# Optimization experiments

Hardware: AMD Instinct MI355X
Metric: run time of the kernel (lower is better)

Reference implementation:

```python
import jax, jax.numpy as jnp
import numpy as np

B, N, E, FIN, H, OUT = 256, 256, 4096, 128, 256, 256
RATIO = 0.5
BN_EPS = 1e-5


def gin_conv(x, src, dst, valid, W1, b1, W2, b2):
    # per-graph: x [n, f], src/dst [E] int, valid [E] bool
    n = x.shape[0]
    v = valid.astype(x.dtype)
    msg = x[jnp.where(valid, src, 0)] * v[:, None]            # [E, f]
    agg = jax.ops.segment_sum(msg, jnp.where(valid, dst, n), num_segments=n + 1)[:n]
    h = x + agg                                               # GINConv eps = 0
    return jax.nn.gelu(h @ W1 + b1) @ W2 + b2


def batch_norm(x, gamma, beta):
    # training-mode BN over all nodes of all graphs: x [B, n, H]
    mean = x.mean(axis=(0, 1))
    var = ((x - mean) ** 2).mean(axis=(0, 1))
    return (x - mean) * jax.lax.rsqrt(var + BN_EPS) * gamma + beta


def topk_pool(x, src, dst, valid, w, k):
    # PyG TopKPooling: score = x.w / ||w||, keep top-k, gate with tanh(score)
    score = (x @ w) / jnp.linalg.norm(w)                      # [n]
    vals, perm = jax.lax.top_k(score, k)
    x_new = x[perm] * jnp.tanh(vals)[:, None]                 # [k, H]
    mapping = jnp.full((x.shape[0],), -1, dtype=jnp.int32).at[perm].set(
        jnp.arange(k, dtype=jnp.int32))
    new_src = mapping[src]
    new_dst = mapping[dst]
    valid_new = valid & (new_src >= 0) & (new_dst >= 0)
    return x_new, new_src, new_dst, valid_new


def block(x, src, dst, valid, W1, b1, W2, b2, gamma, beta, pw):
    x = jax.vmap(gin_conv, in_axes=(0, 0, 0, 0, None, None, None, None))(
        x, src, dst, valid, W1, b1, W2, b2)
    x = jax.nn.gelu(batch_norm(x, gamma, beta))
    k = int(np.ceil(RATIO * x.shape[1]))
    pool = lambda xi, si, di, vi: topk_pool(xi, si, di, vi, pw, k)
    x, src, dst, valid = jax.vmap(pool)(x, src, dst, valid)
    readout = jnp.concatenate([x.max(axis=1), x.mean(axis=1)], axis=-1)  # gmp||gap
    return x, src, dst, valid, readout


def setup_inputs() -> dict:
    key = jax.random.key(0)
    ks = jax.random.split(key, 64)
    d = {}
    d['x'] = jax.random.normal(ks[0], (B, N, FIN), jnp.float32)
    d['edge_index'] = jax.random.randint(ks[1], (B, 2, E), 0, N, dtype=jnp.int32)
    ki = 2
    fin = FIN
    for l in (1, 2, 3, 4):
        d[f'W1_{l}'] = jax.random.normal(ks[ki], (fin, H), jnp.float32) / np.sqrt(fin); ki += 1
        d[f'b1_{l}'] = jnp.zeros((H,), jnp.float32)
        d[f'W2_{l}'] = jax.random.normal(ks[ki], (H, H), jnp.float32) / np.sqrt(H); ki += 1
        d[f'b2_{l}'] = jnp.zeros((H,), jnp.float32)
        d[f'gamma_{l}'] = jnp.ones((H,), jnp.float32)
        d[f'beta_{l}'] = jnp.zeros((H,), jnp.float32)
        d[f'pw_{l}'] = jax.random.normal(ks[ki], (H,), jnp.float32); ki += 1
        fin = H
    d['Wlin'] = jax.random.normal(ks[ki], (2 * H, OUT), jnp.float32) / np.sqrt(2 * H); ki += 1
    d['blin'] = jnp.zeros((OUT,), jnp.float32)
    return d


def reference(x, edge_index,
              W1_1, b1_1, W2_1, b2_1, gamma_1, beta_1, pw_1,
              W1_2, b1_2, W2_2, b2_2, gamma_2, beta_2, pw_2,
              W1_3, b1_3, W2_3, b2_3, gamma_3, beta_3, pw_3,
              W1_4, b1_4, W2_4, b2_4, gamma_4, beta_4, pw_4,
              Wlin, blin):
    src = edge_index[:, 0]
    dst = edge_index[:, 1]
    valid = jnp.ones(src.shape, dtype=bool)
    layers = [
        (W1_1, b1_1, W2_1, b2_1, gamma_1, beta_1, pw_1),
        (W1_2, b1_2, W2_2, b2_2, gamma_2, beta_2, pw_2),
        (W1_3, b1_3, W2_3, b2_3, gamma_3, beta_3, pw_3),
        (W1_4, b1_4, W2_4, b2_4, gamma_4, beta_4, pw_4),
    ]
    total = None
    for p in layers:
        x, src, dst, valid, r = block(x, src, dst, valid, *p)
        total = r if total is None else total + r
    return total @ Wlin + blin
```

## Files before the change

### kernel.cpp

```cpp
#include <hip/hip_runtime.h>
#include <hip/hip_bf16.h>
#include <math.h>

#define BATCH 256
#define NEDGE 4096
#define HDIM 256

typedef __attribute__((ext_vector_type(8))) short short8v;
typedef __attribute__((ext_vector_type(4))) float float4v;

__device__ __forceinline__ float gelu_f(float x) {
  float x3 = x * x * x;
  float t = tanhf(0.7978845608028654f * (x + 0.044715f * x3));
  return 0.5f * x * (1.0f + t);
}

__device__ __forceinline__ void split_bf16(float v, __hip_bfloat16& hi, __hip_bfloat16& lo) {
  hi = __float2bfloat16(v);
  lo = __float2bfloat16(v - __bfloat162float(hi));
}

template<int NN>
__global__ __launch_bounds__(256)
void csr_build_kernel(const int* __restrict__ src_base, int src_stride,
                      const int* __restrict__ dst_base, int dst_stride,
                      int* __restrict__ g_rs,
                      int* __restrict__ g_ids) {
  __shared__ int s_cnt[NN];
  __shared__ int s_rs[NN + 1];
  __shared__ int s_csr[NEDGE];
  const int b = blockIdx.x;
  const int tid = threadIdx.x;
  const int* se = src_base + (size_t)b * src_stride;
  const int* de = dst_base + (size_t)b * dst_stride;
  if (tid < NN) s_cnt[tid] = 0;
  __syncthreads();
  for (int e = tid; e < NEDGE; e += 256) {
    int s = se[e];
    if (s >= 0) atomicAdd(&s_cnt[de[e]], 1);
  }
  __syncthreads();
  if (tid < NN) s_rs[tid] = s_cnt[tid];
  __syncthreads();
  for (int off = 1; off < NN; off <<= 1) {
    int add = 0;
    if (tid < NN && tid >= off) add = s_rs[tid - off];
    __syncthreads();
    if (tid < NN) s_rs[tid] += add;
    __syncthreads();
  }
  int incl = (tid < NN) ? s_rs[tid] : 0;
  __syncthreads();
  if (tid < NN) s_rs[tid + 1] = incl;
  if (tid == 0) s_rs[0] = 0;
  if (tid < NN) s_cnt[tid] = 0;
  __syncthreads();
  for (int e = tid; e < NEDGE; e += 256) {
    int s = se[e];
    if (s >= 0) {
      int d = de[e];
      int p = s_rs[d] + atomicAdd(&s_cnt[d], 1);
      s_csr[p] = s;
    }
  }
  __syncthreads();
  const int total = s_rs[NN];
  for (int i = tid; i <= NN; i += 256) g_rs[b * (NN + 1) + i] = s_rs[i];
  for (int i = tid; i < total; i += 256) g_ids[b * NEDGE + i] = s_csr[i];
}

template<int NN, int FF, int ZS>
__global__ __launch_bounds__(256)
void gin_gather_kernel(const float* __restrict__ x,
                       const int* __restrict__ g_rs, const int* __restrict__ g_ids,
                       __hip_bfloat16* __restrict__ Hhi,
                       __hip_bfloat16* __restrict__ Hlo) {
  constexpr int LPE = 8;
  constexpr int GRP = 256 / LPE;
  constexpr int F4 = FF / 4;
  __shared__ int s_rs[NN + 1];
  __shared__ int s_ids[NEDGE];
  const int b = blockIdx.x;
  const int chunk = blockIdx.y;
  const int tid = threadIdx.x;
  for (int i = tid; i <= NN; i += 256) s_rs[i] = g_rs[b * (NN + 1) + i];
  __syncthreads();
  const int total = s_rs[NN];
  for (int i = tid; i < total; i += 256) s_ids[i] = g_ids[b * NEDGE + i];
  __syncthreads();
  const int lane = tid & (LPE - 1);
  const int grp = tid / LPE;
  const int cb = chunk * LPE;
  const int r0 = blockIdx.z * (NN / ZS);
  const int r1 = r0 + NN / ZS;
  const float4* x4 = (const float4*)x + (size_t)b * NN * F4;
  for (int d = r0 + grp; d < r1; d += GRP) {
    int j0 = s_rs[d], j1 = s_rs[d + 1];
    float4 acc = x4[(size_t)d * F4 + cb + lane];
    for (int j = j0; j < j1; ++j) {
      int s = s_ids[j];
      float4 xv = x4[(size_t)s * F4 + cb + lane];
      acc.x += xv.x; acc.y += xv.y; acc.z += xv.z; acc.w += xv.w;
    }
    float av[4] = {acc.x, acc.y, acc.z, acc.w};
    union { __hip_bfloat16 h[4]; uint2 u; } hv, lv;
#pragma unroll
    for (int j = 0; j < 4; ++j) split_bf16(av[j], hv.h[j], lv.h[j]);
    size_t eo = ((size_t)b * NN + d) * FF + (cb + lane) * 4;
    *(uint2*)&Hhi[eo] = hv.u;
    *(uint2*)&Hlo[eo] = lv.u;
  }
}

template<int K>
__global__ __launch_bounds__(256)
void wsplit_kernel(const float* __restrict__ W,
                   __hip_bfloat16* __restrict__ Whi, __hip_bfloat16* __restrict__ Wlo) {
  int idx = blockIdx.x * 256 + threadIdx.x;
  int c = idx / K, k = idx % K;
  float w = W[(size_t)k * 256 + c];
  __hip_bfloat16 hi, lo;
  split_bf16(w, hi, lo);
  Whi[idx] = hi;
  Wlo[idx] = lo;
}

template<int K, int MODE>
__global__ __launch_bounds__(256)
void mfma_gemm_kernel(const __hip_bfloat16* __restrict__ Ahi,
                      const __hip_bfloat16* __restrict__ Alo,
                      const __hip_bfloat16* __restrict__ Bhi,
                      const __hip_bfloat16* __restrict__ Blo,
                      const float* __restrict__ bias,
                      float* __restrict__ Cf,
                      __hip_bfloat16* __restrict__ Chi,
                      __hip_bfloat16* __restrict__ Clo,
                      float* __restrict__ P1,
                      float* __restrict__ P2) {
  const int tid = threadIdx.x;
  const int wid = tid >> 6, lane = tid & 63;
  const int wr = wid >> 1, wc = wid & 1;
  const int lr = lane & 15, lg = lane >> 4;
  const int rowBase = blockIdx.x * 128 + wr * 64;
  const int colBase = blockIdx.y * 128 + wc * 64;
  float4v acc[4][4];
#pragma unroll
  for (int m = 0; m < 4; ++m)
#pragma unroll
    for (int n = 0; n < 4; ++n) acc[m][n] = (float4v){0.f, 0.f, 0.f, 0.f};
#pragma unroll 2
  for (int k0 = 0; k0 < K; k0 += 32) {
    short8v ah[4], al[4], bh[4], bl[4];
#pragma unroll
    for (int m = 0; m < 4; ++m) {
      size_t off = (size_t)(rowBase + m * 16 + lr) * K + k0 + lg * 8;
      ah[m] = *(const short8v*)(Ahi + off);
      al[m] = *(const short8v*)(Alo + off);
    }
#pragma unroll
    for (int n = 0; n < 4; ++n) {
      size_t off = (size_t)(colBase + n * 16 + lr) * K + k0 + lg * 8;
      bh[n] = *(const short8v*)(Bhi + off);
      bl[n] = *(const short8v*)(Blo + off);
    }
#pragma unroll
    for (int m = 0; m < 4; ++m)
#pragma unroll
      for (int n = 0; n < 4; ++n) {
        acc[m][n] = __builtin_amdgcn_mfma_f32_16x16x32_bf16(ah[m], bh[n], acc[m][n], 0, 0, 0);
        acc[m][n] = __builtin_amdgcn_mfma_f32_16x16x32_bf16(al[m], bh[n], acc[m][n], 0, 0, 0);
        acc[m][n] = __builtin_amdgcn_mfma_f32_16x16x32_bf16(ah[m], bl[n], acc[m][n], 0, 0, 0);
      }
  }
  float s1[4] = {0.f, 0.f, 0.f, 0.f};
  float s2[4] = {0.f, 0.f, 0.f, 0.f};
#pragma unroll
  for (int n = 0; n < 4; ++n) {
    const int col = colBase + n * 16 + lr;
    const float bv = bias[col];
#pragma unroll
    for (int m = 0; m < 4; ++m) {
      const int row0 = rowBase + m * 16 + lg * 4;
#pragma unroll
      for (int i = 0; i < 4; ++i) {
        float o = acc[m][n][i] + bv;
        if (MODE == 1) {
          o = gelu_f(o);
          __hip_bfloat16 hi, lo;
          split_bf16(o, hi, lo);
          Chi[(size_t)(row0 + i) * 256 + col] = hi;
          Clo[(size_t)(row0 + i) * 256 + col] = lo;
        } else {
          Cf[(size_t)(row0 + i) * 256 + col] = o;
          s1[n] += o;
          s2[n] += o * o;
        }
      }
    }
  }
  if constexpr (MODE == 0) {
    __shared__ float r1[128][8];
    __shared__ float r2[128][8];
    const int slot = wr * 4 + lg;
#pragma unroll
    for (int n = 0; n < 4; ++n) {
      const int cidx = wc * 64 + n * 16 + lr;
      r1[cidx][slot] = s1[n];
      r2[cidx][slot] = s2[n];
    }
    __syncthreads();
    if (tid < 128) {
      float a = 0.f, b2 = 0.f;
#pragma unroll
      for (int j = 0; j < 8; ++j) { a += r1[tid][j]; b2 += r2[tid][j]; }
      size_t po = (size_t)blockIdx.x * 256 + blockIdx.y * 128 + tid;
      P1[po] = a;
      P2[po] = b2;
    }
  }
}

__global__ __launch_bounds__(256)
void bn_finalize_kernel(const float* __restrict__ P1, const float* __restrict__ P2,
                        int M, int nblk, const float* __restrict__ pw,
                        float* __restrict__ stats) {
  const int c = blockIdx.x;
  const int tid = threadIdx.x;
  __shared__ double r1[256], r2[256];
  double s = 0.0, s2 = 0.0;
  for (int i = tid; i < nblk; i += 256) {
    s += (double)P1[i * 256 + c];
    s2 += (double)P2[i * 256 + c];
  }
  r1[tid] = s; r2[tid] = s2;
  __syncthreads();
  for (int off = 128; off; off >>= 1) {
    if (tid < off) { r1[tid] += r1[tid + off]; r2[tid] += r2[tid + off]; }
    __syncthreads();
  }
  if (tid == 0) {
    double mean = r1[0] / (double)M;
    double var = r2[0] / (double)M - mean * mean;
    stats[c] = (float)mean;
    stats[256 + c] = (float)(1.0 / sqrt(var + 1e-5));
  }
  if (c == 0) {
    __syncthreads();
    float w = pw[tid];
    r1[tid] = (double)w * (double)w;
    __syncthreads();
    for (int off = 128; off; off >>= 1) {
      if (tid < off) r1[tid] += r1[tid + off];
      __syncthreads();
    }
    if (tid == 0) stats[512] = (float)(1.0 / sqrt(r1[0]));
  }
}

#define SC_ROWS 16
__global__ __launch_bounds__(256)
void score_kernel(const float* __restrict__ y, const float* __restrict__ stats,
                  const float* __restrict__ gamma, const float* __restrict__ beta,
                  const float* __restrict__ pw, float* __restrict__ scores) {
  const int tid = threadIdx.x;
  const int lane = tid & 63, wid = tid >> 6;
  const float4 mean = ((const float4*)stats)[lane];
  const float4 inv = ((const float4*)(stats + 256))[lane];
  const float4 ga = ((const float4*)gamma)[lane];
  const float4 be = ((const float4*)beta)[lane];
  const float4 w = ((const float4*)pw)[lane];
  const float invn = stats[512];
#pragma unroll
  for (int i = 0; i < SC_ROWS / 4; ++i) {
    const int row = blockIdx.x * SC_ROWS + wid + 4 * i;
    float4 v = ((const float4*)y)[(size_t)row * 64 + lane];
    float p = gelu_f((v.x - mean.x) * inv.x * ga.x + be.x) * w.x
            + gelu_f((v.y - mean.y) * inv.y * ga.y + be.y) * w.y
            + gelu_f((v.z - mean.z) * inv.z * ga.z + be.z) * w.z
            + gelu_f((v.w - mean.w) * inv.w * ga.w + be.w) * w.w;
    p *= invn;
#pragma unroll
    for (int off = 32; off; off >>= 1) p += __shfl_xor(p, off, 64);
    if (lane == 0) scores[row] = p;
  }
}

__global__ __launch_bounds__(256)
void topk_kernel(const float* __restrict__ scores,
                 const int* __restrict__ src_in, int src_stride,
                 const int* __restrict__ dst_in, int dst_stride,
                 int* __restrict__ src_out, int* __restrict__ dst_out,
                 int* __restrict__ g_map, float* __restrict__ g_tanh,
                 int n, int k) {
  const int b = blockIdx.x;
  const int tid = threadIdx.x;
  __shared__ float s_sc[256];
  __shared__ int s_map[256];
  if (tid < n) s_sc[tid] = scores[b * n + tid];
  __syncthreads();
  if (tid < n) {
    float si = s_sc[tid];
    int r = 0;
    for (int j = 0; j < n; ++j) {
      float sj = s_sc[j];
      r += (sj > si) || (sj == si && j < tid);
    }
    int m = (r < k) ? r : -1;
    s_map[tid] = m;
    g_map[b * n + tid] = m;
    g_tanh[b * n + tid] = tanhf(si);
  }
  __syncthreads();
  const int* se = src_in + (size_t)b * src_stride;
  const int* de = dst_in + (size_t)b * dst_stride;
  int* so = src_out + (size_t)b * NEDGE;
  int* dq = dst_out + (size_t)b * NEDGE;
  for (int e = tid; e < NEDGE; e += 256) {
    int s = se[e], d = de[e];
    int ns = -1, nd = -1;
    if (s >= 0 && d >= 0) {
      ns = s_map[s];
      nd = s_map[d];
      if (ns < 0 || nd < 0) { ns = -1; nd = -1; }
    }
    so[e] = ns;
    dq[e] = nd;
  }
}

__global__ __launch_bounds__(256)
void pool_gather_kernel(const float* __restrict__ y,
                        const int* __restrict__ g_map, const float* __restrict__ g_tanh,
                        const float* __restrict__ stats, const float* __restrict__ gamma,
                        const float* __restrict__ beta,
                        float* __restrict__ xnext, float* __restrict__ total,
                        int n, int k, int accumulate) {
  const int b = blockIdx.x, chunk = blockIdx.y;
  const int tid = threadIdx.x;
  const int lane = tid & 7;
  const int grp = tid >> 3;
  const int cb = chunk * 8;
  const float4 mean = ((const float4*)stats)[cb + lane];
  const float4 inv = ((const float4*)(stats + 256))[cb + lane];
  const float4 ga = ((const float4*)gamma)[cb + lane];
  const float4 be = ((const float4*)beta)[cb + lane];
  const float4* y4 = (const float4*)y + (size_t)b * n * 64;
  float4* xn4 = (float4*)xnext + (size_t)b * k * 64;
  float4 mx = make_float4(-INFINITY, -INFINITY, -INFINITY, -INFINITY);
  float4 sm = make_float4(0.f, 0.f, 0.f, 0.f);
  for (int i = grp; i < n; i += 32) {
    int r = g_map[b * n + i];
    if (r < 0) continue;
    float tv = g_tanh[b * n + i];
    float4 v = y4[(size_t)i * 64 + cb + lane];
    float4 o;
    o.x = gelu_f((v.x - mean.x) * inv.x * ga.x + be.x) * tv;
    o.y = gelu_f((v.y - mean.y) * inv.y * ga.y + be.y) * tv;
    o.z = gelu_f((v.z - mean.z) * inv.z * ga.z + be.z) * tv;
    o.w = gelu_f((v.w - mean.w) * inv.w * ga.w + be.w) * tv;
    xn4[(size_t)r * 64 + cb + lane] = o;
    mx.x = fmaxf(mx.x, o.x); mx.y = fmaxf(mx.y, o.y);
    mx.z = fmaxf(mx.z, o.z); mx.w = fmaxf(mx.w, o.w);
    sm.x += o.x; sm.y += o.y; sm.z += o.z; sm.w += o.w;
  }
  __shared__ float4 s_mx[256];
  __shared__ float4 s_sm[256];
  s_mx[tid] = mx; s_sm[tid] = sm;
  __syncthreads();
  for (int off = 128; off >= 8; off >>= 1) {
    if (tid < off) {
      float4 a = s_mx[tid], bb = s_mx[tid + off];
      a.x = fmaxf(a.x, bb.x); a.y = fmaxf(a.y, bb.y);
      a.z = fmaxf(a.z, bb.z); a.w = fmaxf(a.w, bb.w);
      s_mx[tid] = a;
      float4 c = s_sm[tid], d = s_sm[tid + off];
      c.x += d.x; c.y += d.y; c.z += d.z; c.w += d.w;
      s_sm[tid] = c;
    }
    __syncthreads();
  }
  if (tid < 8) {
    float4 fmx = s_mx[tid], fsm = s_sm[tid];
    float* tb = total + b * 512;
    const int cbase = chunk * 32 + tid * 4;
    const float invk = 1.f / (float)k;
    float mvals[4] = {fmx.x, fmx.y, fmx.z, fmx.w};
    float svals[4] = {fsm.x, fsm.y, fsm.z, fsm.w};
#pragma unroll
    for (int j = 0; j < 4; ++j) {
      float av = svals[j] * invk;
      if (accumulate) { tb[cbase + j] += mvals[j]; tb[256 + cbase + j] += av; }
      else            { tb[cbase + j] = mvals[j];  tb[256 + cbase + j] = av; }
    }
  }
}

__global__ __launch_bounds__(256)
void final_linear_kernel(const float* __restrict__ total, const float* __restrict__ Wlin,
                         const float* __restrict__ blin, float* __restrict__ out) {
  const int b = blockIdx.x, o = threadIdx.x;
  __shared__ float tl[512];
  tl[o] = total[b * 512 + o];
  tl[256 + o] = total[b * 512 + 256 + o];
  __syncthreads();
  float acc = blin[o];
  for (int cc = 0; cc < 512; ++cc) acc += tl[cc] * Wlin[cc * 256 + o];
  out[b * 256 + o] = acc;
}

template<int NN, int FF>
static void run_layer(const float* xin,
                      const int* src_in, int sstr, const int* dst_in, int dstr,
                      int* src_out, int* dst_out,
                      const float* const* P,
                      int* g_rs, int* g_ids, int* g_map, float* g_tanh,
                      __hip_bfloat16* Ahi, __hip_bfloat16* Alo,
                      __hip_bfloat16* Thi, __hip_bfloat16* Tlo,
                      __hip_bfloat16* W1hi, __hip_bfloat16* W1lo,
                      __hip_bfloat16* W2hi, __hip_bfloat16* W2lo,
                      float* y, float* scores, float* stats,
                      float* P1, float* P2,
                      float* xnext, float* total, int accumulate,
                      hipStream_t stream) {
  constexpr int M = BATCH * NN;
  constexpr int ZS = (NN == 256) ? 2 : 1;
  csr_build_kernel<NN><<<BATCH, 256, 0, stream>>>(src_in, sstr, dst_in, dstr, g_rs, g_ids);
  gin_gather_kernel<NN, FF, ZS><<<dim3(BATCH, FF / 32, ZS), 256, 0, stream>>>(
      xin, g_rs, g_ids, Ahi, Alo);
  wsplit_kernel<FF><<<FF, 256, 0, stream>>>(P[0], W1hi, W1lo);
  wsplit_kernel<256><<<256, 256, 0, stream>>>(P[2], W2hi, W2lo);
  mfma_gemm_kernel<FF, 1><<<dim3(M / 128, 2), 256, 0, stream>>>(
      Ahi, Alo, W1hi, W1lo, P[1], nullptr, Thi, Tlo, nullptr, nullptr);
  mfma_gemm_kernel<256, 0><<<dim3(M / 128, 2), 256, 0, stream>>>(
      Thi, Tlo, W2hi, W2lo, P[3], y, nullptr, nullptr, P1, P2);
  bn_finalize_kernel<<<256, 256, 0, stream>>>(P1, P2, M, M / 128, P[6], stats);
  score_kernel<<<M / SC_ROWS, 256, 0, stream>>>(y, stats, P[4], P[5], P[6], scores);
  topk_kernel<<<BATCH, 256, 0, stream>>>(scores, src_in, sstr, dst_in, dstr,
                                         src_out, dst_out, g_map, g_tanh, NN, NN / 2);
  pool_gather_kernel<<<dim3(BATCH, 8), 256, 0, stream>>>(
      y, g_map, g_tanh, stats, P[4], P[5], xnext, total, NN, NN / 2, accumulate);
}

extern "C" void kernel_launch(void* const* d_in, const int* in_sizes, int n_in,
                              void* d_out, int out_size, void* d_ws, size_t ws_size,
                              hipStream_t stream) {
  (void)in_sizes; (void)n_in; (void)out_size; (void)ws_size;
  const float* x0 = (const float*)d_in[0];
  const int* ei = (const int*)d_in[1];
  const float* Wlin = (const float*)d_in[30];
  const float* blin = (const float*)d_in[31];
  const float* Lp[4][7];
  for (int l = 0; l < 4; ++l)
    for (int j = 0; j < 7; ++j)
      Lp[l][j] = (const float*)d_in[2 + l * 7 + j];

  char* ws = (char*)d_ws;
  size_t off = 0;
  auto alloc = [&](size_t bytes) -> void* {
    void* p = ws + off;
    off += (bytes + 255) & ~(size_t)255;
    return p;
  };
  float* xA = (float*)alloc((size_t)BATCH * 128 * 256 * 4);
  float* y = (float*)alloc((size_t)BATCH * 256 * 256 * 4);
  __hip_bfloat16* Ahi = (__hip_bfloat16*)alloc((size_t)8388608 * 2);
  __hip_bfloat16* Alo = (__hip_bfloat16*)alloc((size_t)8388608 * 2);
  __hip_bfloat16* Thi = (__hip_bfloat16*)alloc((size_t)BATCH * 256 * 256 * 2);
  __hip_bfloat16* Tlo = (__hip_bfloat16*)alloc((size_t)BATCH * 256 * 256 * 2);
  __hip_bfloat16* W1hi = (__hip_bfloat16*)alloc((size_t)256 * 256 * 2);
  __hip_bfloat16* W1lo = (__hip_bfloat16*)alloc((size_t)256 * 256 * 2);
  __hip_bfloat16* W2hi = (__hip_bfloat16*)alloc((size_t)256 * 256 * 2);
  __hip_bfloat16* W2lo = (__hip_bfloat16*)alloc((size_t)256 * 256 * 2);
  float* scores = (float*)alloc((size_t)BATCH * 256 * 4);
  float* stats = (float*)alloc(4096);
  float* P1 = (float*)alloc((size_t)512 * 256 * 4);
  float* P2 = (float*)alloc((size_t)512 * 256 * 4);
  int* es0 = (int*)alloc((size_t)BATCH * NEDGE * 4);
  int* ed0 = (int*)alloc((size_t)BATCH * NEDGE * 4);
  int* es1 = (int*)alloc((size_t)BATCH * NEDGE * 4);
  int* ed1 = (int*)alloc((size_t)BATCH * NEDGE * 4);
  int* g_rs = (int*)alloc((size_t)BATCH * 257 * 4);
  int* g_ids = (int*)alloc((size_t)BATCH * NEDGE * 4);
  int* g_map = (int*)alloc((size_t)BATCH * 256 * 4);
  float* g_tanh = (float*)alloc((size_t)BATCH * 256 * 4);
  float* total = (float*)alloc((size_t)BATCH * 512 * 4);

  run_layer<256, 128>(x0, ei, 2 * NEDGE, ei + NEDGE, 2 * NEDGE, es0, ed0,
                      Lp[0], g_rs, g_ids, g_map, g_tanh,
                      Ahi, Alo, Thi, Tlo, W1hi, W1lo, W2hi, W2lo,
                      y, scores, stats, P1, P2, xA, total, 0, stream);
  run_layer<128, 256>(xA, es0, NEDGE, ed0, NEDGE, es1, ed1,
                      Lp[1], g_rs, g_ids, g_map, g_tanh,
                      Ahi, Alo, Thi, Tlo, W1hi, W1lo, W2hi, W2lo,
                      y, scores, stats, P1, P2, xA, total, 1, stream);
  run_layer<64, 256>(xA, es1, NEDGE, ed1, NEDGE, es0, ed0,
                     Lp[2], g_rs, g_ids, g_map, g_tanh,
                     Ahi, Alo, Thi, Tlo, W1hi, W1lo, W2hi, W2lo,
                     y, scores, stats, P1, P2, xA, total, 1, stream);
  run_layer<32, 256>(xA, es0, NEDGE, ed0, NEDGE, es1, ed1,
                     Lp[3], g_rs, g_ids, g_map, g_tanh,
                     Ahi, Alo, Thi, Tlo, W1hi, W1lo, W2hi, W2lo,
                     y, scores, stats, P1, P2, xA, total, 1, stream);

  final_linear_kernel<<<BATCH, 256, 0, stream>>>(total, Wlin, blin, (float*)d_out);
}
```

Measured before the change: 787.1 us.

## Fuse the two GIN MLP GEMMs into one kernel with the intermediate in LDS

```diff
diff --git a/kernel.cpp b/kernel.cpp
--- a/kernel.cpp
+++ b/kernel.cpp
@@ -125,43 +125,49 @@
   Wlo[idx] = lo;
 }
 
-template<int K, int MODE>
-__global__ __launch_bounds__(256)
-void mfma_gemm_kernel(const __hip_bfloat16* __restrict__ Ahi,
+template<int K1>
+__global__ __launch_bounds__(256)
+void fused_mlp_kernel(const __hip_bfloat16* __restrict__ Ahi,
                       const __hip_bfloat16* __restrict__ Alo,
-                      const __hip_bfloat16* __restrict__ Bhi,
-                      const __hip_bfloat16* __restrict__ Blo,
-                      const float* __restrict__ bias,
-                      float* __restrict__ Cf,
-                      __hip_bfloat16* __restrict__ Chi,
-                      __hip_bfloat16* __restrict__ Clo,
+                      const __hip_bfloat16* __restrict__ B1hi,
+                      const __hip_bfloat16* __restrict__ B1lo,
+                      const float* __restrict__ b1,
+                      const __hip_bfloat16* __restrict__ B2hi,
+                      const __hip_bfloat16* __restrict__ B2lo,
+                      const float* __restrict__ b2,
+                      float* __restrict__ y,
                       float* __restrict__ P1,
                       float* __restrict__ P2) {
-  const int tid = threadIdx.x;
-  const int wid = tid >> 6, lane = tid & 63;
-  const int wr = wid >> 1, wc = wid & 1;
+  constexpr int TSTR = 264;
+  __shared__ __hip_bfloat16 Ths[64 * TSTR];
+  __shared__ __hip_bfloat16 Tls[64 * TSTR];
+  __shared__ float bnr1[256][4];
+  __shared__ float bnr2[256][4];
+  const int tid = threadIdx.x;
+  const int w = tid >> 6, lane = tid & 63;
   const int lr = lane & 15, lg = lane >> 4;
-  const int rowBase = blockIdx.x * 128 + wr * 64;
-  const int colBase = blockIdx.y * 128 + wc * 64;
+  const int rowBase = blockIdx.x * 64;
+  const int colW = w * 64;
   float4v acc[4][4];
+
 #pragma unroll
   for (int m = 0; m < 4; ++m)
 #pragma unroll
     for (int n = 0; n < 4; ++n) acc[m][n] = (float4v){0.f, 0.f, 0.f, 0.f};
 #pragma unroll 2
-  for (int k0 = 0; k0 < K; k0 += 32) {
+  for (int k0 = 0; k0 < K1; k0 += 32) {
     short8v ah[4], al[4], bh[4], bl[4];
 #pragma unroll
     for (int m = 0; m < 4; ++m) {
-      size_t off = (size_t)(rowBase + m * 16 + lr) * K + k0 + lg * 8;
+      size_t off = (size_t)(rowBase + m * 16 + lr) * K1 + k0 + lg * 8;
       ah[m] = *(const short8v*)(Ahi + off);
       al[m] = *(const short8v*)(Alo + off);
     }
 #pragma unroll
     for (int n = 0; n < 4; ++n) {
-      size_t off = (size_t)(colBase + n * 16 + lr) * K + k0 + lg * 8;
-      bh[n] = *(const short8v*)(Bhi + off);
-      bl[n] = *(const short8v*)(Blo + off);
+      size_t off = (size_t)(colW + n * 16 + lr) * K1 + k0 + lg * 8;
+      bh[n] = *(const short8v*)(B1hi + off);
+      bl[n] = *(const short8v*)(B1lo + off);
     }
 #pragma unroll
     for (int m = 0; m < 4; ++m)
@@ -172,51 +178,85 @@
         acc[m][n] = __builtin_amdgcn_mfma_f32_16x16x32_bf16(ah[m], bl[n], acc[m][n], 0, 0, 0);
       }
   }
+#pragma unroll
+  for (int n = 0; n < 4; ++n) {
+    const int col = colW + n * 16 + lr;
+    const float bv = b1[col];
+#pragma unroll
+    for (int m = 0; m < 4; ++m) {
+      const int row = m * 16 + lg * 4;
+#pragma unroll
+      for (int i = 0; i < 4; ++i) {
+        float o = gelu_f(acc[m][n][i] + bv);
+        __hip_bfloat16 hi, lo;
+        split_bf16(o, hi, lo);
+        Ths[(row + i) * TSTR + col] = hi;
+        Tls[(row + i) * TSTR + col] = lo;
+      }
+    }
+  }
+  __syncthreads();
+
+#pragma unroll
+  for (int m = 0; m < 4; ++m)
+#pragma unroll
+    for (int n = 0; n < 4; ++n) acc[m][n] = (float4v){0.f, 0.f, 0.f, 0.f};
+#pragma unroll 2
+  for (int k0 = 0; k0 < 256; k0 += 32) {
+    short8v ah[4], al[4], bh[4], bl[4];
+#pragma unroll
+    for (int m = 0; m < 4; ++m) {
+      const int loff = (m * 16 + lr) * TSTR + k0 + lg * 8;
+      ah[m] = *(const short8v*)(Ths + loff);
+      al[m] = *(const short8v*)(Tls + loff);
+    }
+#pragma unroll
+    for (int n = 0; n < 4; ++n) {
+      size_t off = (size_t)(colW + n * 16 + lr) * 256 + k0 + lg * 8;
+      bh[n] = *(const short8v*)(B2hi + off);
+      bl[n] = *(const short8v*)(B2lo + off);
+    }
+#pragma unroll
+    for (int m = 0; m < 4; ++m)
+#pragma unroll
+      for (int n = 0; n < 4; ++n) {
+        acc[m][n] = __builtin_amdgcn_mfma_f32_16x16x32_bf16(ah[m], bh[n], acc[m][n], 0, 0, 0);
+        acc[m][n] = __builtin_amdgcn_mfma_f32_16x16x32_bf16(al[m], bh[n], acc[m][n], 0, 0, 0);
+        acc[m][n] = __builtin_amdgcn_mfma_f32_16x16x32_bf16(ah[m], bl[n], acc[m][n], 0, 0, 0);
+      }
+  }
   float s1[4] = {0.f, 0.f, 0.f, 0.f};
   float s2[4] = {0.f, 0.f, 0.f, 0.f};
 #pragma unroll
   for (int n = 0; n < 4; ++n) {
-    const int col = colBase + n * 16 + lr;
-    const float bv = bias[col];
+    const int col = colW + n * 16 + lr;
+    const float bv = b2[col];
 #pragma unroll
     for (int m = 0; m < 4; ++m) {
       const int row0 = rowBase + m * 16 + lg * 4;
 #pragma unroll
       for (int i = 0; i < 4; ++i) {
         float o = acc[m][n][i] + bv;
-        if (MODE == 1) {
-          o = gelu_f(o);
-          __hip_bfloat16 hi, lo;
-          split_bf16(o, hi, lo);
-          Chi[(size_t)(row0 + i) * 256 + col] = hi;
-          Clo[(size_t)(row0 + i) * 256 + col] = lo;
-        } else {
-          Cf[(size_t)(row0 + i) * 256 + col] = o;
-          s1[n] += o;
-          s2[n] += o * o;
-        }
+        y[(size_t)(row0 + i) * 256 + col] = o;
+        s1[n] += o;
+        s2[n] += o * o;
       }
     }
   }
-  if constexpr (MODE == 0) {
-    __shared__ float r1[128][8];
-    __shared__ float r2[128][8];
-    const int slot = wr * 4 + lg;
-#pragma unroll
-    for (int n = 0; n < 4; ++n) {
-      const int cidx = wc * 64 + n * 16 + lr;
-      r1[cidx][slot] = s1[n];
-      r2[cidx][slot] = s2[n];
-    }
-    __syncthreads();
-    if (tid < 128) {
-      float a = 0.f, b2 = 0.f;
-#pragma unroll
-      for (int j = 0; j < 8; ++j) { a += r1[tid][j]; b2 += r2[tid][j]; }
-      size_t po = (size_t)blockIdx.x * 256 + blockIdx.y * 128 + tid;
-      P1[po] = a;
-      P2[po] = b2;
-    }
+#pragma unroll
+  for (int n = 0; n < 4; ++n) {
+    const int col = colW + n * 16 + lr;
+    bnr1[col][lg] = s1[n];
+    bnr2[col][lg] = s2[n];
+  }
+  __syncthreads();
+  if (tid < 256) {
+    float a = 0.f, b2s = 0.f;
+#pragma unroll
+    for (int j = 0; j < 4; ++j) { a += bnr1[tid][j]; b2s += bnr2[tid][j]; }
+    size_t po = (size_t)blockIdx.x * 256 + tid;
+    P1[po] = a;
+    P2[po] = b2s;
   }
 }
 
@@ -415,7 +455,6 @@
                       const float* const* P,
                       int* g_rs, int* g_ids, int* g_map, float* g_tanh,
                       __hip_bfloat16* Ahi, __hip_bfloat16* Alo,
-                      __hip_bfloat16* Thi, __hip_bfloat16* Tlo,
                       __hip_bfloat16* W1hi, __hip_bfloat16* W1lo,
                       __hip_bfloat16* W2hi, __hip_bfloat16* W2lo,
                       float* y, float* scores, float* stats,
@@ -429,11 +468,9 @@
       xin, g_rs, g_ids, Ahi, Alo);
   wsplit_kernel<FF><<<FF, 256, 0, stream>>>(P[0], W1hi, W1lo);
   wsplit_kernel<256><<<256, 256, 0, stream>>>(P[2], W2hi, W2lo);
-  mfma_gemm_kernel<FF, 1><<<dim3(M / 128, 2), 256, 0, stream>>>(
-      Ahi, Alo, W1hi, W1lo, P[1], nullptr, Thi, Tlo, nullptr, nullptr);
-  mfma_gemm_kernel<256, 0><<<dim3(M / 128, 2), 256, 0, stream>>>(
-      Thi, Tlo, W2hi, W2lo, P[3], y, nullptr, nullptr, P1, P2);
-  bn_finalize_kernel<<<256, 256, 0, stream>>>(P1, P2, M, M / 128, P[6], stats);
+  fused_mlp_kernel<FF><<<M / 64, 256, 0, stream>>>(
+      Ahi, Alo, W1hi, W1lo, P[1], W2hi, W2lo, P[3], y, P1, P2);
+  bn_finalize_kernel<<<256, 256, 0, stream>>>(P1, P2, M, M / 64, P[6], stats);
   score_kernel<<<M / SC_ROWS, 256, 0, stream>>>(y, stats, P[4], P[5], P[6], scores);
   topk_kernel<<<BATCH, 256, 0, stream>>>(scores, src_in, sstr, dst_in, dstr,
                                          src_out, dst_out, g_map, g_tanh, NN, NN / 2);
@@ -465,16 +502,14 @@
   float* y = (float*)alloc((size_t)BATCH * 256 * 256 * 4);
   __hip_bfloat16* Ahi = (__hip_bfloat16*)alloc((size_t)8388608 * 2);
   __hip_bfloat16* Alo = (__hip_bfloat16*)alloc((size_t)8388608 * 2);
-  __hip_bfloat16* Thi = (__hip_bfloat16*)alloc((size_t)BATCH * 256 * 256 * 2);
-  __hip_bfloat16* Tlo = (__hip_bfloat16*)alloc((size_t)BATCH * 256 * 256 * 2);
   __hip_bfloat16* W1hi = (__hip_bfloat16*)alloc((size_t)256 * 256 * 2);
   __hip_bfloat16* W1lo = (__hip_bfloat16*)alloc((size_t)256 * 256 * 2);
   __hip_bfloat16* W2hi = (__hip_bfloat16*)alloc((size_t)256 * 256 * 2);
   __hip_bfloat16* W2lo = (__hip_bfloat16*)alloc((size_t)256 * 256 * 2);
   float* scores = (float*)alloc((size_t)BATCH * 256 * 4);
   float* stats = (float*)alloc(4096);
-  float* P1 = (float*)alloc((size_t)512 * 256 * 4);
-  float* P2 = (float*)alloc((size_t)512 * 256 * 4);
+  float* P1 = (float*)alloc((size_t)1024 * 256 * 4);
+  float* P2 = (float*)alloc((size_t)1024 * 256 * 4);
   int* es0 = (int*)alloc((size_t)BATCH * NEDGE * 4);
   int* ed0 = (int*)alloc((size_t)BATCH * NEDGE * 4);
   int* es1 = (int*)alloc((size_t)BATCH * NEDGE * 4);
@@ -487,19 +522,19 @@
 
   run_layer<256, 128>(x0, ei, 2 * NEDGE, ei + NEDGE, 2 * NEDGE, es0, ed0,
                       Lp[0], g_rs, g_ids, g_map, g_tanh,
-                      Ahi, Alo, Thi, Tlo, W1hi, W1lo, W2hi, W2lo,
+                      Ahi, Alo, W1hi, W1lo, W2hi, W2lo,
                       y, scores, stats, P1, P2, xA, total, 0, stream);
   run_layer<128, 256>(xA, es0, NEDGE, ed0, NEDGE, es1, ed1,
                       Lp[1], g_rs, g_ids, g_map, g_tanh,
-                      Ahi, Alo, Thi, Tlo, W1hi, W1lo, W2hi, W2lo,
+                      Ahi, Alo, W1hi, W1lo, W2hi, W2lo,
                       y, scores, stats, P1, P2, xA, total, 1, stream);
   run_layer<64, 256>(xA, es1, NEDGE, ed1, NEDGE, es0, ed0,
                      Lp[2], g_rs, g_ids, g_map, g_tanh,
-                     Ahi, Alo, Thi, Tlo, W1hi, W1lo, W2hi, W2lo,
+                     Ahi, Alo, W1hi, W1lo, W2hi, W2lo,
                      y, scores, stats, P1, P2, xA, total, 1, stream);
   run_layer<32, 256>(xA, es0, NEDGE, ed0, NEDGE, es1, ed1,
                      Lp[3], g_rs, g_ids, g_map, g_tanh,
-                     Ahi, Alo, Thi, Tlo, W1hi, W1lo, W2hi, W2lo,
+                     Ahi, Alo, W1hi, W1lo, W2hi, W2lo,
                      y, scores, stats, P1, P2, xA, total, 1, stream);
 
   final_linear_kernel<<<BATCH, 256, 0, stream>>>(total, Wlin, blin, (float*)d_out);
```

Measured after the change: 688.0 us. 1.14x faster.
